# Performance work log

Measured on AMD Instinct MI355X. Metric: run time of the kernel, lower is better.

Reference implementation:

```python
import jax, jax.numpy as jnp
import numpy as np

B, NA, T, NV, D = 24, 50, 10, 196, 512


def setup_inputs() -> dict:
    key = jax.random.key(0)
    k1, k2 = jax.random.split(key)
    return {
        "audio_feats": jax.random.normal(k1, (B, NA, D), dtype=jnp.float32),
        "visual_feats": jax.random.normal(k2, (B, T, NV, D), dtype=jnp.float32),
        "temperature": jnp.float32(2.5),
        "scale_factor": jnp.float32(2.5),
        "threshold": jnp.float32(-2.5),
    }


def _l2norm(x):
    # F.normalize(dim=-1): x / max(||x||, 1e-12)
    n = jnp.sqrt(jnp.sum(x * x, axis=-1, keepdims=True))
    return x / jnp.maximum(n, 1e-12)


def reference(audio_feats, visual_feats, temperature, scale_factor, threshold):
    b = audio_feats.shape[0]
    a = _l2norm(audio_feats)          # (B,Na,D)
    v = _l2norm(visual_feats)         # (B,T,Nv,D)
    # all-pairs token similarities: (B,B,Na,T,Nv)
    sims = jnp.einsum('xad,ytvd->xyatv', a, v) / temperature

    # aggregate_temporal_similarities
    th = jax.nn.sigmoid(threshold)
    max_vis = jnp.max(sims, axis=-1)            # (B,B,Na,T)
    raw_diff = max_vis - th
    sel = jax.nn.relu(raw_diff) * scale_factor  # selection strength
    weighted_sum = jnp.sum(max_vis * sel, axis=-1)   # over T
    weights_sum = jnp.sum(sel, axis=-1)
    token_sims = weighted_sum / jnp.maximum(weights_sum, 1e-6)
    clip_sims = jnp.mean(token_sims, axis=-1)   # (B,B)
    fraction_selected = jnp.mean((raw_diff > 0).astype(jnp.float32))

    # InfoNCE
    idx = jnp.arange(b)
    losses_a2v = -jax.nn.log_softmax(clip_sims, axis=1)[idx, idx]
    losses_v2a = -jax.nn.log_softmax(clip_sims.T, axis=1)[idx, idx]
    contrastive_loss = jnp.mean(losses_a2v + losses_v2a) / 2

    # regularization
    neg = jnp.clip(sims, -20.0, 0.0)
    l_nonneg = jnp.mean(neg * neg)
    temp_low = jnp.maximum(-jnp.log(temperature), 0.0) ** 2   # log(1)=0
    temp_high = jnp.maximum(jnp.log(temperature) - jnp.log(4.0), 0.0) ** 2
    l_cal = temp_low + temp_high
    l_threshold = jnp.maximum(th - 0.9, 0.0) ** 2 + jnp.maximum(0.1 - th, 0.0) ** 2
    l_scale = jnp.maximum(scale_factor - 20.0, 0.0) ** 2 + jnp.maximum(1.0 - scale_factor, 0.0) ** 2
    reg_loss = 0.15 * l_nonneg + 2.0 * l_cal + 0.1 * l_threshold + 0.1 * l_scale

    # selection reward on positive pairs (diagonal)
    pos_diffs = raw_diff[idx, idx]                       # (B,Na,T)
    sel_ratio = (jnp.tanh(20.0 * pos_diffs) + 1.0) / 2.0
    selection_reward = -0.1 * jnp.log1p(jnp.mean(sel_ratio))

    total_loss = selection_reward + contrastive_loss + reg_loss
    return (total_loss, contrastive_loss, reg_loss, fraction_selected, selection_reward)
```

## Files before the change

### kernel.cpp

```cpp
#include <hip/hip_runtime.h>
#include <math.h>

#define B_   24
#define NA_  50
#define T_   10
#define NV_  196
#define D_   512
#define M_   1200
#define MPAD 1280
#define NVP  224
#define YT_  240
#define VROWS (YT_ * NVP)
#define ABLK 320

typedef __bf16 bf16x8 __attribute__((ext_vector_type(8)));
typedef float  f32x4  __attribute__((ext_vector_type(4)));
typedef unsigned short ushort8 __attribute__((ext_vector_type(8)));

__device__ __forceinline__ unsigned short f2bf(float f) {
    unsigned u = __float_as_uint(f);
    u += 0x7FFF + ((u >> 16) & 1);
    return (unsigned short)(u >> 16);
}

__device__ __forceinline__ void gload16(const void* g, void* l) {
    __builtin_amdgcn_global_load_lds(
        (const __attribute__((address_space(1))) unsigned int*)g,
        (__attribute__((address_space(3))) unsigned int*)l, 16, 0, 0);
}

__global__ void normconv_kernel(const float* __restrict__ a,
                                const float* __restrict__ vf,
                                const float* __restrict__ tempPtr,
                                unsigned short* __restrict__ Abf,
                                unsigned short* __restrict__ Vbf,
                                float* __restrict__ accs) {
    if (blockIdx.x == 0 && threadIdx.x < 4) accs[threadIdx.x] = 0.0f;
    int w = threadIdx.x >> 6, lane = threadIdx.x & 63;
    int bid = blockIdx.x;
    const float* src = nullptr;
    ushort8* dst;
    float tscale = 1.0f;
    if (bid < ABLK) {
        int row = bid * 4 + w;
        dst = (ushort8*)(Abf + (size_t)row * D_ + lane * 8);
        if (row < M_) { src = a + (size_t)row * D_ + lane * 8; tscale = tempPtr[0]; }
    } else {
        int row = (bid - ABLK) * 4 + w;
        dst = (ushort8*)(Vbf + (size_t)row * D_ + lane * 8);
        int yt = row / NVP, vv = row - yt * NVP;
        if (vv < NV_) src = vf + ((size_t)yt * NV_ + vv) * D_ + lane * 8;
    }
    if (src) {
        float4 u = *(const float4*)src;
        float4 v = *(const float4*)(src + 4);
        float s = u.x*u.x + u.y*u.y + u.z*u.z + u.w*u.w
                + v.x*v.x + v.y*v.y + v.z*v.z + v.w*v.w;
        #pragma unroll
        for (int off = 32; off; off >>= 1) s += __shfl_xor(s, off, 64);
        float sc = 1.0f / (fmaxf(sqrtf(s), 1e-12f) * tscale);
        ushort8 o;
        o[0]=f2bf(u.x*sc); o[1]=f2bf(u.y*sc); o[2]=f2bf(u.z*sc); o[3]=f2bf(u.w*sc);
        o[4]=f2bf(v.x*sc); o[5]=f2bf(v.y*sc); o[6]=f2bf(v.z*sc); o[7]=f2bf(v.w*sc);
        *dst = o;
    } else {
        ushort8 z = (ushort8)0;
        *dst = z;
    }
}

__global__ __launch_bounds__(512) void simred_kernel(
    const unsigned short* __restrict__ Abf, const unsigned short* __restrict__ Vbf,
    float* __restrict__ maxvis, float* __restrict__ accNonneg)
{
    __shared__ __align__(16) unsigned char lds[16384 + 14336];
    __shared__ float maxred[2][256];
    __shared__ float redbuf[8];

    const int tid  = threadIdx.x;
    const int lane = tid & 63;
    const int w    = tid >> 6;
    const int lrow = lane >> 2;
    const int lcol = lane & 3;
    const int q    = lane >> 4;
    const int m16  = lane & 15;
    const int wr   = w & 3;
    const int wc   = w >> 2;

    const int lin = blockIdx.y * gridDim.x + blockIdx.x;
    const int swz = (lin & 7) * 150 + (lin >> 3);
    const int bx  = swz % 5;
    const int yt  = swz / 5;
    const int rowA0 = bx * 256;
    const size_t vRow0 = (size_t)yt * NVP;

    const int scol = lcol ^ ((lrow >> 1) & 3);
    const unsigned short* gp[4];
    const unsigned char*  lp[4];
    int nun = 0;
    for (int u = w; u < 30; u += 8) {
        if (u < 16) gp[nun] = Abf + ((size_t)(rowA0 + u * 16 + lrow)) * D_ + scol * 8;
        else        gp[nun] = Vbf + (vRow0 + (size_t)((u - 16) * 16 + lrow)) * D_ + scol * 8;
        lp[nun] = lds + u * 1024;
        ++nun;
    }

    const unsigned rsw = (unsigned)((m16 >> 1) & 3) * 16u;
    unsigned aoff[4], boff[7];
    #pragma unroll
    for (int i = 0; i < 4; ++i)
        aoff[i] = (unsigned)(wr * 64 + i * 16 + m16) * 64u + (((unsigned)q * 16u) ^ rsw);
    #pragma unroll
    for (int j = 0; j < 7; ++j)
        boff[j] = 16384u + (unsigned)(wc * 112 + j * 16 + m16) * 64u + (((unsigned)q * 16u) ^ rsw);

    f32x4 acc[4][7];
    #pragma unroll
    for (int i = 0; i < 4; ++i)
        #pragma unroll
        for (int j = 0; j < 7; ++j) acc[i][j] = (f32x4)0.0f;

    for (int c = 0; c < 16; ++c) {
        const int kc = c * 32;
        __syncthreads();
        #pragma unroll 4
        for (int i = 0; i < 4; ++i)
            if (i < nun) gload16(gp[i] + kc, (void*)lp[i]);
        __syncthreads();
        bf16x8 af[4], bfr[7];
        #pragma unroll
        for (int i = 0; i < 4; ++i) af[i] = *(const bf16x8*)(lds + aoff[i]);
        #pragma unroll
        for (int j = 0; j < 7; ++j) bfr[j] = *(const bf16x8*)(lds + boff[j]);
        #pragma unroll
        for (int i = 0; i < 4; ++i)
            #pragma unroll
            for (int j = 0; j < 7; ++j)
                acc[i][j] = __builtin_amdgcn_mfma_f32_16x16x32_bf16(af[i], bfr[j], acc[i][j], 0, 0, 0);
    }

    float cs = 0.0f;
    #pragma unroll
    for (int i = 0; i < 4; ++i)
        #pragma unroll
        for (int j = 0; j < 7; ++j)
            #pragma unroll
            for (int r = 0; r < 4; ++r) {
                float v = acc[i][j][r];
                float cv = fminf(fmaxf(v, -20.0f), 0.0f);
                cs += cv * cv;
            }
    #pragma unroll
    for (int off = 32; off; off >>= 1) cs += __shfl_xor(cs, off, 64);
    if (lane == 0) redbuf[w] = cs;

    bool colv[7];
    #pragma unroll
    for (int j = 0; j < 7; ++j) colv[j] = (wc * 112 + j * 16 + m16) < NV_;
    #pragma unroll
    for (int i = 0; i < 4; ++i) {
        float mx[4] = {-3e38f, -3e38f, -3e38f, -3e38f};
        #pragma unroll
        for (int j = 0; j < 7; ++j)
            #pragma unroll
            for (int r = 0; r < 4; ++r)
                mx[r] = fmaxf(mx[r], colv[j] ? acc[i][j][r] : -3e38f);
        #pragma unroll
        for (int r = 0; r < 4; ++r) {
            float mm = mx[r];
            #pragma unroll
            for (int off = 1; off <= 8; off <<= 1) mm = fmaxf(mm, __shfl_xor(mm, off, 64));
            if (m16 == 0) maxred[wc][wr * 64 + i * 16 + q * 4 + r] = mm;
        }
    }
    __syncthreads();
    if (tid == 0) atomicAdd(accNonneg, redbuf[0] + redbuf[1] + redbuf[2] + redbuf[3]
                                     + redbuf[4] + redbuf[5] + redbuf[6] + redbuf[7]);
    if (tid < 256) {
        float mm = fmaxf(maxred[0][tid], maxred[1][tid]);
        int R = rowA0 + tid;
        if (R < M_) {
            int x = R / NA_, a = R - x * NA_;
            int y = yt / T_, t = yt - y * T_;
            maxvis[(((size_t)x * B_ + y) * NA_ + a) * T_ + t] = mm;
        }
    }
}

__global__ void aggfin_kernel(const float* __restrict__ maxvis,
                              const float* __restrict__ thrPtr,
                              const float* __restrict__ scalePtr,
                              const float* __restrict__ tempPtr,
                              float* __restrict__ clipSims,
                              float* __restrict__ accs,
                              float* __restrict__ out)
{
    int xy = blockIdx.x;
    int x = xy / B_, y = xy % B_;
    int a = threadIdx.x;
    float th    = 1.0f / (1.0f + expf(-thrPtr[0]));
    float scale = scalePtr[0];
    float token = 0.0f, cnt = 0.0f, selsum = 0.0f;
    if (a < NA_) {
        const float* p = maxvis + (((size_t)x * B_ + y) * NA_ + a) * T_;
        float ws = 0.0f, ss = 0.0f;
        #pragma unroll
        for (int t = 0; t < T_; ++t) {
            float mv  = p[t];
            float rd  = mv - th;
            float sel = fmaxf(rd, 0.0f) * scale;
            ws += mv * sel;
            ss += sel;
            if (rd > 0.0f) cnt += 1.0f;
            if (x == y) selsum += 0.5f * (tanhf(20.0f * rd) + 1.0f);
        }
        token = ws / fmaxf(ss, 1e-6f);
    }
    #pragma unroll
    for (int off = 32; off; off >>= 1) {
        token  += __shfl_xor(token,  off, 64);
        cnt    += __shfl_xor(cnt,    off, 64);
        selsum += __shfl_xor(selsum, off, 64);
    }
    if (threadIdx.x == 0) {
        clipSims[x * B_ + y] = token / (float)NA_;
        atomicAdd(&accs[1], cnt);
        if (x == y) atomicAdd(&accs[2], selsum);
    }
    __threadfence();
    unsigned last = 0;
    if (threadIdx.x == 0) {
        unsigned v = atomicAdd((unsigned int*)(accs + 3), 1u);
        last = ((v % (unsigned)(B_ * B_)) == (unsigned)(B_ * B_ - 1));
    }
    last = __shfl((int)last, 0, 64);
    if (!last) return;
    __threadfence();

    __shared__ float cs[B_ * B_];
    int tid = threadIdx.x;
    for (int i = tid; i < B_ * B_; i += 64) cs[i] = clipSims[i];
    __syncthreads();
    float lsum = 0.0f;
    if (tid < B_) {
        int i = tid;
        float m = -1e30f;
        for (int j = 0; j < B_; ++j) m = fmaxf(m, cs[i * B_ + j]);
        float e = 0.0f;
        for (int j = 0; j < B_; ++j) e += expf(cs[i * B_ + j] - m);
        float la = m + logf(e) - cs[i * B_ + i];
        float m2 = -1e30f;
        for (int j = 0; j < B_; ++j) m2 = fmaxf(m2, cs[j * B_ + i]);
        float e2 = 0.0f;
        for (int j = 0; j < B_; ++j) e2 += expf(cs[j * B_ + i] - m2);
        float lv = m2 + logf(e2) - cs[i * B_ + i];
        lsum = la + lv;
    }
    #pragma unroll
    for (int off = 32; off; off >>= 1) lsum += __shfl_xor(lsum, off, 64);
    if (tid == 0) {
        float contrastive = lsum / (float)B_ * 0.5f;
        float temp = tempPtr[0], scl = scalePtr[0];
        float l_nonneg = accs[0] / 56448000.0f;
        float logt = logf(temp);
        float tl  = fmaxf(-logt, 0.0f);
        float thi = fmaxf(logt - logf(4.0f), 0.0f);
        float l_cal = tl * tl + thi * thi;
        float t1 = fmaxf(th - 0.9f, 0.0f), t2 = fmaxf(0.1f - th, 0.0f);
        float l_thr = t1 * t1 + t2 * t2;
        float s1 = fmaxf(scl - 20.0f, 0.0f), s2 = fmaxf(1.0f - scl, 0.0f);
        float l_scale = s1 * s1 + s2 * s2;
        float reg = 0.15f * l_nonneg + 2.0f * l_cal + 0.1f * l_thr + 0.1f * l_scale;
        float frac   = accs[1] / 288000.0f;
        float selrew = -0.1f * log1pf(accs[2] / 12000.0f);
        out[0] = selrew + contrastive + reg;
        out[1] = contrastive;
        out[2] = reg;
        out[3] = frac;
        out[4] = selrew;
    }
}

extern "C" void kernel_launch(void* const* d_in, const int* in_sizes, int n_in,
                              void* d_out, int out_size, void* d_ws, size_t ws_size,
                              hipStream_t stream) {
    const float* audio  = (const float*)d_in[0];
    const float* visual = (const float*)d_in[1];
    const float* temp   = (const float*)d_in[2];
    const float* scale  = (const float*)d_in[3];
    const float* thr    = (const float*)d_in[4];
    float* out = (float*)d_out;

    unsigned char* wsb = (unsigned char*)d_ws;
    unsigned short* Abf = (unsigned short*)wsb;
    unsigned short* Vbf = (unsigned short*)(wsb + 1310720);
    float* maxvis   = (float*)(wsb + 1310720 + 55050240);
    float* clipSims = (float*)(wsb + 1310720 + 55050240 + 1152000);
    float* accs     = clipSims + 576;

    normconv_kernel<<<ABLK + VROWS / 4, 256, 0, stream>>>(audio, visual, temp, Abf, Vbf, accs);

    dim3 grid(MPAD / 256, YT_);
    simred_kernel<<<grid, 512, 0, stream>>>(Abf, Vbf, maxvis, accs);

    aggfin_kernel<<<B_ * B_, 64, 0, stream>>>(maxvis, thr, scale, temp, clipSims, accs, out);
}
```

Before: 295.7 us.

## Double-buffer LDS in simred GEMM with async prefetch two chunks ahead

```diff
diff --git a/kernel.cpp b/kernel.cpp
--- a/kernel.cpp
+++ b/kernel.cpp
@@ -12,6 +12,10 @@
 #define YT_  240
 #define VROWS (YT_ * NVP)
 #define ABLK 320
+
+#define NT    16
+#define BUFB  32768u
+#define VBASE 16384u
 
 typedef __bf16 bf16x8 __attribute__((ext_vector_type(8)));
 typedef float  f32x4  __attribute__((ext_vector_type(4)));
@@ -69,13 +73,13 @@
     }
 }
 
-__global__ __launch_bounds__(512) void simred_kernel(
+__global__ __launch_bounds__(512, 1) void simred_kernel(
     const unsigned short* __restrict__ Abf, const unsigned short* __restrict__ Vbf,
     float* __restrict__ maxvis, float* __restrict__ accNonneg)
 {
-    __shared__ __align__(16) unsigned char lds[16384 + 14336];
-    __shared__ float maxred[2][256];
-    __shared__ float redbuf[8];
+    __shared__ __align__(16) unsigned char lds[2 * BUFB];
+    float* maxredp = (float*)(lds + 30720);
+    float* redbufp = (float*)(lds + BUFB + 30720);
 
     const int tid  = threadIdx.x;
     const int lane = tid & 63;
@@ -96,13 +100,14 @@
 
     const int scol = lcol ^ ((lrow >> 1) & 3);
     const unsigned short* gp[4];
-    const unsigned char*  lp[4];
-    int nun = 0;
-    for (int u = w; u < 30; u += 8) {
-        if (u < 16) gp[nun] = Abf + ((size_t)(rowA0 + u * 16 + lrow)) * D_ + scol * 8;
-        else        gp[nun] = Vbf + (vRow0 + (size_t)((u - 16) * 16 + lrow)) * D_ + scol * 8;
-        lp[nun] = lds + u * 1024;
-        ++nun;
+    unsigned loff[4];
+    #pragma unroll
+    for (int k = 0; k < 4; ++k) {
+        int u = w + 8 * k;
+        if (u < 16)      gp[k] = Abf + ((size_t)(rowA0 + u * 16 + lrow)) * D_ + scol * 8;
+        else if (u < 30) gp[k] = Vbf + (vRow0 + (size_t)((u - 16) * 16 + lrow)) * D_ + scol * 8;
+        else             gp[k] = Abf + (size_t)lane * 8;
+        loff[k] = (unsigned)u * 1024u;
     }
 
     const unsigned rsw = (unsigned)((m16 >> 1) & 3) * 16u;
@@ -112,7 +117,7 @@
         aoff[i] = (unsigned)(wr * 64 + i * 16 + m16) * 64u + (((unsigned)q * 16u) ^ rsw);
     #pragma unroll
     for (int j = 0; j < 7; ++j)
-        boff[j] = 16384u + (unsigned)(wc * 112 + j * 16 + m16) * 64u + (((unsigned)q * 16u) ^ rsw);
+        boff[j] = VBASE + (unsigned)(wc * 112 + j * 16 + m16) * 64u + (((unsigned)q * 16u) ^ rsw);
 
     f32x4 acc[4][7];
     #pragma unroll
@@ -120,23 +125,38 @@
         #pragma unroll
         for (int j = 0; j < 7; ++j) acc[i][j] = (f32x4)0.0f;
 
-    for (int c = 0; c < 16; ++c) {
-        const int kc = c * 32;
-        __syncthreads();
-        #pragma unroll 4
+    #pragma unroll
+    for (int k = 0; k < 4; ++k) gload16(gp[k], (void*)(lds + loff[k]));
+    #pragma unroll
+    for (int k = 0; k < 4; ++k) gload16(gp[k] + 32, (void*)(lds + BUFB + loff[k]));
+    asm volatile("s_waitcnt vmcnt(4)\ns_barrier" ::: "memory");
+
+    #pragma unroll 2
+    for (int t = 0; t < NT; ++t) {
+        const unsigned char* buf = lds + (unsigned)(t & 1) * BUFB;
+        bf16x8 af[4], bv[7];
+        #pragma unroll
+        for (int i = 0; i < 4; ++i) af[i] = *(const bf16x8*)(buf + aoff[i]);
+        #pragma unroll
+        for (int j = 0; j < 7; ++j) bv[j] = *(const bf16x8*)(buf + boff[j]);
+        asm volatile("s_waitcnt lgkmcnt(0)\ns_barrier" ::: "memory");
+        __builtin_amdgcn_sched_barrier(0);
+        if (t < NT - 2) {
+            const int kc2 = (t + 2) * 32;
+            #pragma unroll
+            for (int k = 0; k < 4; ++k)
+                gload16(gp[k] + kc2, (void*)(lds + (unsigned)(t & 1) * BUFB + loff[k]));
+        }
+        __builtin_amdgcn_sched_barrier(0);
+        __builtin_amdgcn_s_setprio(1);
+        #pragma unroll
         for (int i = 0; i < 4; ++i)
-            if (i < nun) gload16(gp[i] + kc, (void*)lp[i]);
-        __syncthreads();
-        bf16x8 af[4], bfr[7];
-        #pragma unroll
-        for (int i = 0; i < 4; ++i) af[i] = *(const bf16x8*)(lds + aoff[i]);
-        #pragma unroll
-        for (int j = 0; j < 7; ++j) bfr[j] = *(const bf16x8*)(lds + boff[j]);
-        #pragma unroll
-        for (int i = 0; i < 4; ++i)
             #pragma unroll
             for (int j = 0; j < 7; ++j)
-                acc[i][j] = __builtin_amdgcn_mfma_f32_16x16x32_bf16(af[i], bfr[j], acc[i][j], 0, 0, 0);
+                acc[i][j] = __builtin_amdgcn_mfma_f32_16x16x32_bf16(af[i], bv[j], acc[i][j], 0, 0, 0);
+        __builtin_amdgcn_s_setprio(0);
+        if (t < NT - 2)       asm volatile("s_waitcnt vmcnt(4)\ns_barrier" ::: "memory");
+        else if (t == NT - 2) asm volatile("s_waitcnt vmcnt(0)\ns_barrier" ::: "memory");
     }
 
     float cs = 0.0f;
@@ -152,7 +172,7 @@
             }
     #pragma unroll
     for (int off = 32; off; off >>= 1) cs += __shfl_xor(cs, off, 64);
-    if (lane == 0) redbuf[w] = cs;
+    if (lane == 0) redbufp[w] = cs;
 
     bool colv[7];
     #pragma unroll
@@ -170,14 +190,14 @@
             float mm = mx[r];
             #pragma unroll
             for (int off = 1; off <= 8; off <<= 1) mm = fmaxf(mm, __shfl_xor(mm, off, 64));
-            if (m16 == 0) maxred[wc][wr * 64 + i * 16 + q * 4 + r] = mm;
+            if (m16 == 0) maxredp[wc * 256 + wr * 64 + i * 16 + q * 4 + r] = mm;
         }
     }
     __syncthreads();
-    if (tid == 0) atomicAdd(accNonneg, redbuf[0] + redbuf[1] + redbuf[2] + redbuf[3]
-                                     + redbuf[4] + redbuf[5] + redbuf[6] + redbuf[7]);
+    if (tid == 0) atomicAdd(accNonneg, redbufp[0] + redbufp[1] + redbufp[2] + redbufp[3]
+                                     + redbufp[4] + redbufp[5] + redbufp[6] + redbufp[7]);
     if (tid < 256) {
-        float mm = fmaxf(maxred[0][tid], maxred[1][tid]);
+        float mm = fmaxf(maxredp[tid], maxredp[256 + tid]);
         int R = rowA0 + tid;
         if (R < M_) {
             int x = R / NA_, a = R - x * NA_;
```

New measurement: 277.4 us. -6.2%, faster.
